# Kernel optimization log

Measured on AMD Instinct MI355X. Metric: run time of the kernel, lower is better.

The kernel has to match this reference:

```python
import jax, jax.numpy as jnp
import numpy as np

R = 6            # search radius
P = 2 * R + 1    # patch size = 13
D = 4            # mask downsample rate
TOPK = 36        # top-k over patch dim (eval path)


def _corr(fq, fm):
    """Local correlation volume (SpatialCorrelationSampler, kernel=1, patch=P).
    fq, fm: [b,c,h,w] -> [b, P*P, h*w]."""
    b, c, h, w = fq.shape
    fmp = jnp.pad(fm, ((0, 0), (0, 0), (R, R), (R, R)))
    rows = []
    for di in range(P):
        for dj in range(P):
            rows.append(jnp.einsum('bchw,bchw->bhw', fq, fmp[:, :, di:di + h, dj:dj + w]))
    return jnp.stack(rows, 1).reshape(b, P * P, h * w)


def _unfold(msk):
    """F.unfold(msk, kernel_size=P, padding=R): [b,o,h,w] -> [b,o,P*P,h*w]."""
    b, o, h, w = msk.shape
    mp = jnp.pad(msk, ((0, 0), (0, 0), (R, R), (R, R)))
    pats = [mp[:, :, di:di + h, dj:dj + w] for di in range(P) for dj in range(P)]
    return jnp.stack(pats, 2).reshape(b, o, P * P, h * w)


def _forward(feat_query, feat_mem0, feat_mem1, msk_mem0, msk_mem1):
    b, c, h, w = feat_query.shape
    # correlation volumes for each memory frame, concat over patch dim
    corr = jnp.concatenate([_corr(feat_query, feat_mem0),
                            _corr(feat_query, feat_mem1)], axis=1)
    corr = corr / jnp.sqrt(jnp.asarray(c, corr.dtype))          # [b, 2*P*P, N]
    # eval path: top-k over the (frames*P*P) patch axis, per pixel
    corr_t = corr.transpose(0, 2, 1)                              # [b, N, 2PP]
    vals, idx = jax.lax.top_k(corr_t, TOPK)                       # [b, N, K]
    wts = jax.nn.softmax(vals, axis=-1)                           # [b, N, K]
    # downsample masks by strided slicing, unfold, concat over patch dim
    msk = jnp.concatenate([_unfold(msk_mem0[:, :, ::D, ::D]),
                           _unfold(msk_mem1[:, :, ::D, ::D])], axis=2)  # [b,o,2PP,N]
    msk_t = msk.transpose(0, 3, 1, 2)                             # [b, N, o, 2PP]
    g = jnp.take_along_axis(msk_t, idx[:, :, None, :], axis=3)    # [b, N, o, K]
    out = (wts[:, :, None, :] * g).sum(-1)                        # [b, N, o]
    obj = msk_mem0.shape[1]
    return out.transpose(0, 2, 1).reshape(b, obj, h, w)


def setup_inputs() -> dict:
    key = jax.random.key(0)
    k = jax.random.split(key, 5)
    b, c, h, w = 1, 256, 120, 216
    obj = 11
    return {
        'feat_query': jax.random.normal(k[0], (b, c, h, w), jnp.float32),
        'feat_mem0': jax.random.normal(k[1], (b, c, h, w), jnp.float32),
        'feat_mem1': jax.random.normal(k[2], (b, c, h, w), jnp.float32),
        'msk_mem0': jax.random.uniform(k[3], (b, obj, h * D, w * D), jnp.float32),
        'msk_mem1': jax.random.uniform(k[4], (b, obj, h * D, w * D), jnp.float32),
    }


def reference(feat_query, feat_mem0, feat_mem1, msk_mem0, msk_mem1):
    return _forward(feat_query, feat_mem0, feat_mem1, msk_mem0, msk_mem1)
```

## Files before the change

kernel.cpp:

```cpp
#include <hip/hip_runtime.h>
#include <hip/hip_bf16.h>
#include <math.h>

#define H 120
#define W 216
#define C 256
#define NPIX (H*W)
#define PATCH 13
#define PP 169
#define RAD 6
#define TOPKN 36
#define OBJ 11
#define MD 4
#define CW 344

typedef unsigned short ushort;
typedef unsigned int   uint;
typedef __attribute__((ext_vector_type(8))) __bf16 bf16x8;
typedef __attribute__((ext_vector_type(4))) float   f32x4;

#define PLANE_B ((size_t)NPIX * 512)

#define YT 8
#define RT 20
#define XT 16
#define UW 32
#define PXS 128
#define ROWS (UW * PXS)
#define BUFB (RT * ROWS)
#define NXT 14
#define NYT 15
#define NWG (NXT * 2 * NYT)

__device__ inline ushort f2bf_rne(float x) {
  uint u = __float_as_uint(x);
  uint r = (u + 0x7FFFu + ((u >> 16) & 1u)) >> 16;
  return (ushort)r;
}
__device__ inline float bf2f(ushort h) { return __uint_as_float(((uint)h) << 16); }

__global__ __launch_bounds__(256) void k_prep(const float* __restrict__ fq,
                      const float* __restrict__ fm0, const float* __restrict__ fm1,
                      char* fqt, char* fm0t, char* fm1t) {
  const float* src = (blockIdx.z == 0) ? fq : (blockIdx.z == 1) ? fm0 : fm1;
  char* dst = (blockIdx.z == 0) ? fqt : (blockIdx.z == 1) ? fm0t : fm1t;

  const int p0 = blockIdx.x * 64;
  const int c0 = blockIdx.y * 64;
  const int tid = threadIdx.x;

  __shared__ float ts[64 * 65];
  {
    int p = tid & 63, cl = tid >> 6;
    #pragma unroll
    for (int jj = 0; jj < 16; ++jj) {
      int c = 4 * jj + cl;
      ts[c * 65 + p] = src[(size_t)(c0 + c) * NPIX + p0 + p];
    }
  }
  __syncthreads();
  {
    int pl = tid >> 2, sub = tid & 3;
    ushort hb[16], lb[16];
    #pragma unroll
    for (int i = 0; i < 16; ++i) {
      float x = ts[(sub * 16 + i) * 65 + pl];
      ushort h = f2bf_rne(x);
      hb[i] = h;
      lb[i] = f2bf_rne(x - bf2f(h));
    }
    size_t off = (size_t)(p0 + pl) * 512 + (size_t)c0 * 2 + sub * 32;
    *(uint4*)(dst + off)            = ((uint4*)hb)[0];
    *(uint4*)(dst + off + 16)       = ((uint4*)hb)[1];
    *(uint4*)(dst + PLANE_B + off)      = ((uint4*)lb)[0];
    *(uint4*)(dst + PLANE_B + off + 16) = ((uint4*)lb)[1];
  }
}

__global__ void k_downsample(const float* __restrict__ m0, const float* __restrict__ m1,
                             float* __restrict__ mds) {
  int i = blockIdx.x * 256 + threadIdx.x;
  const int total = 2 * OBJ * NPIX;
  if (i >= total) return;
  int fo = i / NPIX;
  int pix = i - fo * NPIX;
  int f = fo / OBJ, o = fo - f * OBJ;
  int y = pix / W, x = pix - y * W;
  const float* src = f ? m1 : m0;
  mds[i] = src[(size_t)o * (H*MD) * (W*MD) + (size_t)(MD*y) * (W*MD) + MD*x];
}

__global__ __launch_bounds__(1024, 4) void k_corr_mfma(const char* __restrict__ fqt,
                        const char* __restrict__ fm0t, const char* __restrict__ fm1t,
                        float* __restrict__ corr) {
  int b = blockIdx.x;
  int xcd = b & 7;
  int wgid = ((xcd < 4) ? xcd * 53 : 4 * 53 + (xcd - 4) * 52) + (b >> 3);
  int yt   = wgid % NYT;
  int rest = wgid / NYT;
  int f    = rest & 1;
  int xt   = rest >> 1;

  const int y0 = yt * YT;
  const int X0 = xt * XT;
  const int tid  = threadIdx.x;
  const int wv   = tid >> 6;
  const int wyy  = wv >> 1;
  const int nt   = wv & 1;
  const int lane = tid & 63;
  const int l15  = lane & 15, l4 = lane >> 4;
  const int y    = y0 + wyy;

  const char* frame = f ? fm1t : fm0t;

  __shared__ __align__(16) char bsm[2 * BUFB];

  const char* gsrc[5];
  #pragma unroll
  for (int i = 0; i < 5; ++i) {
    int gdest = wv * 64 + lane + 1024 * i;
    int ri  = gdest >> 8;
    int rem = gdest & 255;
    int px  = rem >> 3;
    int pqp = rem & 7;
    int pqs = pqp ^ (px & 7);
    int p   = pqs >> 2, q = pqs & 3;
    int r = y0 - 6 + ri;  r = (r < 0) ? 0 : (r >= H ? H - 1 : r);
    int u = X0 - 8 + px;  u = (u < 0) ? 0 : (u >= W ? W - 1 : u);
    gsrc[i] = frame + (size_t)p * PLANE_B + (size_t)(r * W + u) * 512 + q * 16;
  }

  int xA = X0 + l15;
  const char* pa = fqt + (size_t)(y * W + (xA < W ? xA : W - 1)) * 512 + l4 * 16;

  const int pxn = 16 * nt + l15;
  const uint sw  = (uint)((l15 & 7) << 4);
  const uint bh_off = (uint)((pxn * PXS +      l4 * 16) ^ sw);
  const uint bl_off = (uint)((pxn * PXS + 64 + l4 * 16) ^ sw);

  int u0 = X0 + 16 * nt + l15 - 8;
  bool uok = (u0 >= 0) && (u0 < W);

  f32x4 acc[13];
  #pragma unroll
  for (int di = 0; di < 13; ++di) acc[di] = (f32x4){0.f, 0.f, 0.f, 0.f};

  auto STAGE = [&](int buf, int kc) {
    #pragma unroll
    for (int i = 0; i < 5; ++i)
      __builtin_amdgcn_global_load_lds(
        (const __attribute__((address_space(1))) void*)(gsrc[i] + kc * 64),
        (__attribute__((address_space(3))) void*)(bsm + buf * BUFB + wv * 1024 + i * 16384),
        16, 0, 0);
  };

  STAGE(0, 0);
  uint4 aCh = *(const uint4*)(pa);
  uint4 aCl = *(const uint4*)(pa + PLANE_B);
  uint4 aNh, aNl;
  __syncthreads();

  #pragma unroll
  for (int kc = 0; kc < 8; ++kc) {
    if (kc < 7) {
      STAGE((kc + 1) & 1, kc + 1);
      aNh = *(const uint4*)(pa + (kc + 1) * 64);
      aNl = *(const uint4*)(pa + PLANE_B + (kc + 1) * 64);
    }
    const char* bb = bsm + (kc & 1) * BUFB;
    bf16x8 Ahv = __builtin_bit_cast(bf16x8, aCh);
    bf16x8 Alv = __builtin_bit_cast(bf16x8, aCl);

    #pragma unroll
    for (int di = 0; di < 13; ++di) {
      int rr = y + di - RAD;
      if (rr >= 0 && rr < H) {
        const char* rb = bb + (wyy + di) * ROWS;
        bf16x8 Bhv = *(const bf16x8*)(rb + bh_off);
        bf16x8 Blv = *(const bf16x8*)(rb + bl_off);
        acc[di] = __builtin_amdgcn_mfma_f32_16x16x32_bf16(Ahv, Bhv, acc[di], 0, 0, 0);
        acc[di] = __builtin_amdgcn_mfma_f32_16x16x32_bf16(Ahv, Blv, acc[di], 0, 0, 0);
        acc[di] = __builtin_amdgcn_mfma_f32_16x16x32_bf16(Alv, Bhv, acc[di], 0, 0, 0);
      }
    }
    aCh = aNh; aCl = aNl;
    __syncthreads();
  }

  float* cb = corr + (size_t)(y * W) * CW + f * PP;
  #pragma unroll
  for (int di = 0; di < 13; ++di) {
    #pragma unroll
    for (int j = 0; j < 4; ++j) {
      int m  = l4 * 4 + j;
      int x  = X0 + m;
      int dj = 16 * nt + l15 - m - 2;
      if (x < W && dj >= 0 && dj < PATCH)
        cb[(size_t)x * CW + di * PATCH + dj] = uok ? acc[di][j] * 0.0625f : 0.f;
    }
  }
}

__global__ __launch_bounds__(64) void k_corr_valu(const float* __restrict__ fq,
                       const float* __restrict__ fm0, const float* __restrict__ fm1,
                       float* __restrict__ corr) {
  int b = blockIdx.x;
  int lb = (b & 7) * 390 + (b >> 3);
  int y   = lb / 26;
  int r26 = lb - y * 26;
  int f   = r26 / 13;
  int di  = r26 - f * 13;
  const int tid = threadIdx.x;
  const int xg  = tid;
  const int r   = y + di - RAD;

  float* corr_base = corr + (size_t)(y * W) * CW + (f * PP + di * PATCH);

  if (r < 0 || r >= H) {
    if (xg < 54) {
      float* cp = corr_base + (size_t)(4 * xg) * CW;
      #pragma unroll
      for (int sub = 0; sub < 4; ++sub) {
        #pragma unroll
        for (int dj = 0; dj < PATCH; ++dj) cp[(size_t)sub * CW + dj] = 0.f;
      }
    }
    return;
  }

  const float* fm = f ? fm1 : fm0;
  __shared__ float fm_s[4 * 232];

  const float* pf[4];
  int  ldsoff[4];
  bool sval[4], mval[4];
  #pragma unroll
  for (int s = 0; s < 4; ++s) {
    int i = tid + 64 * s;
    sval[s] = (i < 232);
    int ii = sval[s] ? i : 0;
    int ch = ii / 58;
    int m  = ii - ch * 58;
    int x  = 4 * m - 8;
    mval[s] = sval[s] && (m >= 2) && (m <= 55);
    ldsoff[s] = ch * 232 + 4 * m;
    pf[s] = fm + (size_t)ch * NPIX + (size_t)r * W + (mval[s] ? x : 0);
  }

  const float* pq = fq + (size_t)y * W + 4 * ((xg < 54) ? xg : 0);

  float4 acc[PATCH];
  #pragma unroll
  for (int d = 0; d < PATCH; ++d) acc[d] = make_float4(0.f, 0.f, 0.f, 0.f);

  for (int c0 = 0; c0 < C; c0 += 4) {
    #pragma unroll
    for (int s = 0; s < 4; ++s) {
      if (sval[s]) {
        float4 v = make_float4(0.f, 0.f, 0.f, 0.f);
        if (mval[s]) v = *(const float4*)(pf[s]);
        *(float4*)&fm_s[ldsoff[s]] = v;
        pf[s] += 4 * (size_t)NPIX;
      }
    }
    __syncthreads();
    if (xg < 54) {
      #pragma unroll
      for (int ch = 0; ch < 4; ++ch) {
        float4 q4 = *(const float4*)(pq + (size_t)ch * NPIX);
        float rv[20];
        #pragma unroll
        for (int qq = 0; qq < 5; ++qq) {
          float4 t4 = *(const float4*)&fm_s[ch * 232 + 4 * xg + 4 * qq];
          rv[4*qq+0] = t4.x; rv[4*qq+1] = t4.y; rv[4*qq+2] = t4.z; rv[4*qq+3] = t4.w;
        }
        #pragma unroll
        for (int dj = 0; dj < PATCH; ++dj) {
          acc[dj].x += q4.x * rv[dj + 2];
          acc[dj].y += q4.y * rv[dj + 3];
          acc[dj].z += q4.z * rv[dj + 4];
          acc[dj].w += q4.w * rv[dj + 5];
        }
      }
      pq += 4 * (size_t)NPIX;
    }
    __syncthreads();
  }

  if (xg < 54) {
    float* cp = corr_base + (size_t)(4 * xg) * CW;
    #pragma unroll
    for (int dj = 0; dj < PATCH; ++dj) {
      cp[dj]                  = acc[dj].x * 0.0625f;
      cp[(size_t)1 * CW + dj] = acc[dj].y * 0.0625f;
      cp[(size_t)2 * CW + dj] = acc[dj].z * 0.0625f;
      cp[(size_t)3 * CW + dj] = acc[dj].w * 0.0625f;
    }
  }
}

__global__ __launch_bounds__(256) void k_topk(const float* __restrict__ corr,
                       const float* __restrict__ mds, float* __restrict__ out) {
  int wid = (blockIdx.x * 256 + threadIdx.x) >> 6;
  int lane = threadIdx.x & 63;
  if (wid >= NPIX) return;
  const float* cr = corr + (size_t)wid * CW;

  float v[6]; uint ui[6];
  #pragma unroll
  for (int s = 0; s < 6; ++s) {
    int idx = lane + 64 * s;
    bool ok = idx < 2 * PP;
    float f = ok ? cr[idx] : 0.f;
    v[s] = f;
    uint bb = __float_as_uint(f);
    uint u = bb ^ (uint)(((int)bb >> 31) | 0x80000000);
    ui[s] = ok ? u : 0u;
  }

  uint blo = 0u, bhi = 0xFFFFFFFFu;
  for (int it = 0; it < 32; ++it) {
    uint mid = blo + ((bhi - blo) >> 1);
    int c = 0;
    #pragma unroll
    for (int s = 0; s < 6; ++s)
      c += __popcll(__ballot(ui[s] > mid));
    if (c <= 35) bhi = mid; else blo = mid + 1;
  }
  const uint x0 = blo;

  int c_gt = 0;
  #pragma unroll
  for (int s = 0; s < 6; ++s) c_gt += __popcll(__ballot(ui[s] > x0));
  const int need = 36 - c_gt;

  uint tb = (x0 & 0x80000000u) ? (x0 ^ 0x80000000u) : ~x0;
  const float tf = __uint_as_float(tb);

  float w[6];
  float zp = 0.f;
  int prior = 0;
  #pragma unroll
  for (int s = 0; s < 6; ++s) {
    unsigned long long tie = __ballot(ui[s] == x0);
    uint below = __builtin_amdgcn_mbcnt_hi((uint)(tie >> 32),
                  __builtin_amdgcn_mbcnt_lo((uint)tie, 0u));
    bool acc = (ui[s] > x0) || ((ui[s] == x0) && ((prior + (int)below) < need));
    prior += __popcll(tie);
    w[s] = acc ? __expf(v[s] - tf) : 0.f;
    zp += w[s];
  }
  float Z = zp;
  #pragma unroll
  for (int off = 32; off >= 1; off >>= 1) Z += __shfl_xor(Z, off, 64);

  int y = wid / W, x = wid - (wid / W) * W;
  float no[OBJ];
  #pragma unroll
  for (int o = 0; o < OBJ; ++o) no[o] = 0.f;
  #pragma unroll
  for (int s = 0; s < 6; ++s) {
    if (w[s] > 0.f) {
      int idx = lane + 64 * s;
      int ff = idx >= PP;
      int r = idx - ff * PP;
      int di = r / PATCH, dj = r - (r / PATCH) * PATCH;
      int yy = y + di - RAD, xx = x + dj - RAD;
      if (yy >= 0 && yy < H && xx >= 0 && xx < W) {
        const float* mb = mds + ((size_t)ff * OBJ) * NPIX + yy * W + xx;
        #pragma unroll
        for (int o = 0; o < OBJ; ++o) no[o] += w[s] * mb[(size_t)o * NPIX];
      }
    }
  }
  float inv = 1.f / Z;
  #pragma unroll
  for (int o = 0; o < OBJ; ++o) {
    float p = no[o];
    #pragma unroll
    for (int off = 32; off >= 1; off >>= 1) p += __shfl_xor(p, off, 64);
    if (lane == 0) out[(size_t)o * NPIX + wid] = p * inv;
  }
}

extern "C" void kernel_launch(void* const* d_in, const int* in_sizes, int n_in,
                              void* d_out, int out_size, void* d_ws, size_t ws_size,
                              hipStream_t stream) {
  const float* fq  = (const float*)d_in[0];
  const float* fm0 = (const float*)d_in[1];
  const float* fm1 = (const float*)d_in[2];
  const float* m0  = (const float*)d_in[3];
  const float* m1  = (const float*)d_in[4];
  float* out = (float*)d_out;

  char* ws = (char*)d_ws;
  size_t off = 0;
  auto alloc = [&](size_t sz) { size_t o = off; off = (off + sz + 1023) & ~(size_t)1023; return o; };

  size_t mds_o  = alloc((size_t)2 * OBJ * NPIX * sizeof(float));
  size_t corr_o = alloc((size_t)NPIX * CW * sizeof(float));
  size_t fqt_o  = alloc(2 * PLANE_B);
  size_t fm0t_o = alloc(2 * PLANE_B);
  size_t fm1t_o = alloc(2 * PLANE_B);
  size_t needed = off;

  float* mds  = (float*)(ws + mds_o);
  float* corr = (float*)(ws + corr_o);

  k_downsample<<<(2 * OBJ * NPIX + 255) / 256, 256, 0, stream>>>(m0, m1, mds);

  if (ws_size >= needed) {
    char* fqt  = ws + fqt_o;
    char* fm0t = ws + fm0t_o;
    char* fm1t = ws + fm1t_o;
    dim3 gp(405, 4, 3);
    k_prep<<<gp, 256, 0, stream>>>(fq, fm0, fm1, fqt, fm0t, fm1t);
    k_corr_mfma<<<NWG, 1024, 0, stream>>>(fqt, fm0t, fm1t, corr);
  } else {
    k_corr_valu<<<120 * 26, 64, 0, stream>>>(fq, fm0, fm1, corr);
  }

  k_topk<<<NPIX / 4, 256, 0, stream>>>(corr, mds, out);
}
```

Before: 134.1 us.

## Compute two query rows per wave in correlation MFMA kernel to reuse B loads

Each wave now handles two adjacent query rows instead of one, so the block shrinks from 1024 to 512 threads. Every B fragment read from LDS for one memory row feeds both accumulator sets, which cuts LDS reads per MFMA roughly in half. Each wave also issues twice as many global-to-LDS staging loads. The cost is double the accumulator registers (26 f32x4), lower occupancy via launch bounds (512,2), and fewer waves per block to hide latency.

```diff
diff --git a/kernel.cpp b/kernel.cpp
--- a/kernel.cpp
+++ b/kernel.cpp
@@ -90,7 +90,7 @@
   mds[i] = src[(size_t)o * (H*MD) * (W*MD) + (size_t)(MD*y) * (W*MD) + MD*x];
 }
 
-__global__ __launch_bounds__(1024, 4) void k_corr_mfma(const char* __restrict__ fqt,
+__global__ __launch_bounds__(512, 2) void k_corr_mfma(const char* __restrict__ fqt,
                         const char* __restrict__ fm0t, const char* __restrict__ fm1t,
                         float* __restrict__ corr) {
   int b = blockIdx.x;
@@ -105,33 +105,34 @@
   const int X0 = xt * XT;
   const int tid  = threadIdx.x;
   const int wv   = tid >> 6;
-  const int wyy  = wv >> 1;
+  const int p    = wv >> 1;
   const int nt   = wv & 1;
   const int lane = tid & 63;
   const int l15  = lane & 15, l4 = lane >> 4;
-  const int y    = y0 + wyy;
+  const int ya   = y0 + 2 * p;
 
   const char* frame = f ? fm1t : fm0t;
 
   __shared__ __align__(16) char bsm[2 * BUFB];
 
-  const char* gsrc[5];
-  #pragma unroll
-  for (int i = 0; i < 5; ++i) {
-    int gdest = wv * 64 + lane + 1024 * i;
+  const char* gsrc[10];
+  #pragma unroll
+  for (int i = 0; i < 10; ++i) {
+    int gdest = wv * 640 + i * 64 + lane;
     int ri  = gdest >> 8;
     int rem = gdest & 255;
     int px  = rem >> 3;
     int pqp = rem & 7;
     int pqs = pqp ^ (px & 7);
-    int p   = pqs >> 2, q = pqs & 3;
+    int pp  = pqs >> 2, q = pqs & 3;
     int r = y0 - 6 + ri;  r = (r < 0) ? 0 : (r >= H ? H - 1 : r);
     int u = X0 - 8 + px;  u = (u < 0) ? 0 : (u >= W ? W - 1 : u);
-    gsrc[i] = frame + (size_t)p * PLANE_B + (size_t)(r * W + u) * 512 + q * 16;
+    gsrc[i] = frame + (size_t)pp * PLANE_B + (size_t)(r * W + u) * 512 + q * 16;
   }
 
   int xA = X0 + l15;
-  const char* pa = fqt + (size_t)(y * W + (xA < W ? xA : W - 1)) * 512 + l4 * 16;
+  const char* pa0 = fqt + (size_t)(ya * W + (xA < W ? xA : W - 1)) * 512 + l4 * 16;
+  const char* pa1 = pa0 + (size_t)W * 512;
 
   const int pxn = 16 * nt + l15;
   const uint sw  = (uint)((l15 & 7) << 4);
@@ -141,53 +142,70 @@
   int u0 = X0 + 16 * nt + l15 - 8;
   bool uok = (u0 >= 0) && (u0 < W);
 
-  f32x4 acc[13];
-  #pragma unroll
-  for (int di = 0; di < 13; ++di) acc[di] = (f32x4){0.f, 0.f, 0.f, 0.f};
+  f32x4 acc0[13], acc1[13];
+  #pragma unroll
+  for (int di = 0; di < 13; ++di) {
+    acc0[di] = (f32x4){0.f, 0.f, 0.f, 0.f};
+    acc1[di] = (f32x4){0.f, 0.f, 0.f, 0.f};
+  }
 
   auto STAGE = [&](int buf, int kc) {
     #pragma unroll
-    for (int i = 0; i < 5; ++i)
+    for (int i = 0; i < 10; ++i)
       __builtin_amdgcn_global_load_lds(
         (const __attribute__((address_space(1))) void*)(gsrc[i] + kc * 64),
-        (__attribute__((address_space(3))) void*)(bsm + buf * BUFB + wv * 1024 + i * 16384),
+        (__attribute__((address_space(3))) void*)(bsm + buf * BUFB + wv * 10240 + i * 1024),
         16, 0, 0);
   };
 
   STAGE(0, 0);
-  uint4 aCh = *(const uint4*)(pa);
-  uint4 aCl = *(const uint4*)(pa + PLANE_B);
-  uint4 aNh, aNl;
+  uint4 aC0h = *(const uint4*)(pa0);
+  uint4 aC0l = *(const uint4*)(pa0 + PLANE_B);
+  uint4 aC1h = *(const uint4*)(pa1);
+  uint4 aC1l = *(const uint4*)(pa1 + PLANE_B);
+  uint4 aN0h, aN0l, aN1h, aN1l;
   __syncthreads();
 
   #pragma unroll
   for (int kc = 0; kc < 8; ++kc) {
     if (kc < 7) {
       STAGE((kc + 1) & 1, kc + 1);
-      aNh = *(const uint4*)(pa + (kc + 1) * 64);
-      aNl = *(const uint4*)(pa + PLANE_B + (kc + 1) * 64);
+      aN0h = *(const uint4*)(pa0 + (kc + 1) * 64);
+      aN0l = *(const uint4*)(pa0 + PLANE_B + (kc + 1) * 64);
+      aN1h = *(const uint4*)(pa1 + (kc + 1) * 64);
+      aN1l = *(const uint4*)(pa1 + PLANE_B + (kc + 1) * 64);
     }
     const char* bb = bsm + (kc & 1) * BUFB;
-    bf16x8 Ahv = __builtin_bit_cast(bf16x8, aCh);
-    bf16x8 Alv = __builtin_bit_cast(bf16x8, aCl);
-
-    #pragma unroll
-    for (int di = 0; di < 13; ++di) {
-      int rr = y + di - RAD;
-      if (rr >= 0 && rr < H) {
-        const char* rb = bb + (wyy + di) * ROWS;
+    bf16x8 A0h = __builtin_bit_cast(bf16x8, aC0h);
+    bf16x8 A0l = __builtin_bit_cast(bf16x8, aC0l);
+    bf16x8 A1h = __builtin_bit_cast(bf16x8, aC1h);
+    bf16x8 A1l = __builtin_bit_cast(bf16x8, aC1l);
+
+    #pragma unroll
+    for (int ri = 0; ri < 14; ++ri) {
+      int row = ya + ri - RAD;
+      if (row >= 0 && row < H) {
+        const char* rb = bb + (2 * p + ri) * ROWS;
         bf16x8 Bhv = *(const bf16x8*)(rb + bh_off);
         bf16x8 Blv = *(const bf16x8*)(rb + bl_off);
-        acc[di] = __builtin_amdgcn_mfma_f32_16x16x32_bf16(Ahv, Bhv, acc[di], 0, 0, 0);
-        acc[di] = __builtin_amdgcn_mfma_f32_16x16x32_bf16(Ahv, Blv, acc[di], 0, 0, 0);
-        acc[di] = __builtin_amdgcn_mfma_f32_16x16x32_bf16(Alv, Bhv, acc[di], 0, 0, 0);
-      }
-    }
-    aCh = aNh; aCl = aNl;
+        if (ri <= 12) {
+          acc0[ri] = __builtin_amdgcn_mfma_f32_16x16x32_bf16(A0h, Bhv, acc0[ri], 0, 0, 0);
+          acc0[ri] = __builtin_amdgcn_mfma_f32_16x16x32_bf16(A0h, Blv, acc0[ri], 0, 0, 0);
+          acc0[ri] = __builtin_amdgcn_mfma_f32_16x16x32_bf16(A0l, Bhv, acc0[ri], 0, 0, 0);
+        }
+        if (ri >= 1) {
+          acc1[ri-1] = __builtin_amdgcn_mfma_f32_16x16x32_bf16(A1h, Bhv, acc1[ri-1], 0, 0, 0);
+          acc1[ri-1] = __builtin_amdgcn_mfma_f32_16x16x32_bf16(A1h, Blv, acc1[ri-1], 0, 0, 0);
+          acc1[ri-1] = __builtin_amdgcn_mfma_f32_16x16x32_bf16(A1l, Bhv, acc1[ri-1], 0, 0, 0);
+        }
+      }
+    }
+    aC0h = aN0h; aC0l = aN0l; aC1h = aN1h; aC1l = aN1l;
     __syncthreads();
   }
 
-  float* cb = corr + (size_t)(y * W) * CW + f * PP;
+  float* cb0 = corr + (size_t)(ya * W) * CW + f * PP;
+  float* cb1 = cb0 + (size_t)W * CW;
   #pragma unroll
   for (int di = 0; di < 13; ++di) {
     #pragma unroll
@@ -195,8 +213,10 @@
       int m  = l4 * 4 + j;
       int x  = X0 + m;
       int dj = 16 * nt + l15 - m - 2;
-      if (x < W && dj >= 0 && dj < PATCH)
-        cb[(size_t)x * CW + di * PATCH + dj] = uok ? acc[di][j] * 0.0625f : 0.f;
+      if (x < W && dj >= 0 && dj < PATCH) {
+        cb0[(size_t)x * CW + di * PATCH + dj] = uok ? acc0[di][j] * 0.0625f : 0.f;
+        cb1[(size_t)x * CW + di * PATCH + dj] = uok ? acc1[di][j] * 0.0625f : 0.f;
+      }
     }
   }
 }
@@ -376,10 +396,10 @@
   float inv = 1.f / Z;
   #pragma unroll
   for (int o = 0; o < OBJ; ++o) {
-    float p = no[o];
-    #pragma unroll
-    for (int off = 32; off >= 1; off >>= 1) p += __shfl_xor(p, off, 64);
-    if (lane == 0) out[(size_t)o * NPIX + wid] = p * inv;
+    float pr = no[o];
+    #pragma unroll
+    for (int off = 32; off >= 1; off >>= 1) pr += __shfl_xor(pr, off, 64);
+    if (lane == 0) out[(size_t)o * NPIX + wid] = pr * inv;
   }
 }
 
@@ -415,7 +435,7 @@
     char* fm1t = ws + fm1t_o;
     dim3 gp(405, 4, 3);
     k_prep<<<gp, 256, 0, stream>>>(fq, fm0, fm1, fqt, fm0t, fm1t);
-    k_corr_mfma<<<NWG, 1024, 0, stream>>>(fqt, fm0t, fm1t, corr);
+    k_corr_mfma<<<NWG, 512, 0, stream>>>(fqt, fm0t, fm1t, corr);
   } else {
     k_corr_valu<<<120 * 26, 64, 0, stream>>>(fq, fm0, fm1, corr);
   }
```

Measured after the change: 138.3 us. 1.03x slower.

## Process both memory frames per workgroup and use two-stage radix top-k threshold search

Applied to the files above, without the earlier changes.

The correlation kernel now loops over both memory frames inside one workgroup, halving the grid to 210 workgroups. It pipelines the frame-1 staging behind the frame-0 compute and reuses the query A-operand addressing. The XCD remapping is adjusted for the smaller grid. The top-k kernel first does a 16-iteration binary search on the upper 16 bits of the key and only falls back to a full-precision refinement when ties straddle the threshold, cutting the per-pixel ballot loop count in the common case. Risks are lower occupancy and parallelism for the correlation stage (210 blocks across 256 CUs) and divergence in the fallback path.

```diff
diff --git a/kernel.cpp b/kernel.cpp
--- a/kernel.cpp
+++ b/kernel.cpp
@@ -30,7 +30,7 @@
 #define BUFB (RT * ROWS)
 #define NXT 14
 #define NYT 15
-#define NWG (NXT * 2 * NYT)
+#define NWG2 (NXT * NYT)
 
 __device__ inline ushort f2bf_rne(float x) {
   uint u = __float_as_uint(x);
@@ -94,12 +94,10 @@
                         const char* __restrict__ fm0t, const char* __restrict__ fm1t,
                         float* __restrict__ corr) {
   int b = blockIdx.x;
-  int xcd = b & 7;
-  int wgid = ((xcd < 4) ? xcd * 53 : 4 * 53 + (xcd - 4) * 52) + (b >> 3);
+  int xcd = b & 7, idx = b >> 3;
+  int wgid = (xcd < 2) ? xcd * 27 + idx : 54 + (xcd - 2) * 26 + idx;
   int yt   = wgid % NYT;
-  int rest = wgid / NYT;
-  int f    = rest & 1;
-  int xt   = rest >> 1;
+  int xt   = wgid / NYT;
 
   const int y0 = yt * YT;
   const int X0 = xt * XT;
@@ -111,11 +109,12 @@
   const int l15  = lane & 15, l4 = lane >> 4;
   const int y    = y0 + wyy;
 
-  const char* frame = f ? fm1t : fm0t;
-
   __shared__ __align__(16) char bsm[2 * BUFB];
 
-  const char* gsrc[5];
+  uint soff[5];
+  uint ldst;
+  {
+  }
   #pragma unroll
   for (int i = 0; i < 5; ++i) {
     int gdest = wv * 64 + lane + 1024 * i;
@@ -127,8 +126,9 @@
     int p   = pqs >> 2, q = pqs & 3;
     int r = y0 - 6 + ri;  r = (r < 0) ? 0 : (r >= H ? H - 1 : r);
     int u = X0 - 8 + px;  u = (u < 0) ? 0 : (u >= W ? W - 1 : u);
-    gsrc[i] = frame + (size_t)p * PLANE_B + (size_t)(r * W + u) * 512 + q * 16;
-  }
+    soff[i] = (uint)((size_t)p * PLANE_B + (size_t)(r * W + u) * 512 + q * 16);
+  }
+  ldst = (uint)(wv * 1024 + lane * 16);
 
   int xA = X0 + l15;
   const char* pa = fqt + (size_t)(y * W + (xA < W ? xA : W - 1)) * 512 + l4 * 16;
@@ -145,58 +145,65 @@
   #pragma unroll
   for (int di = 0; di < 13; ++di) acc[di] = (f32x4){0.f, 0.f, 0.f, 0.f};
 
-  auto STAGE = [&](int buf, int kc) {
+  auto STAGE = [&](int buf, const char* fb, int kn) {
     #pragma unroll
     for (int i = 0; i < 5; ++i)
       __builtin_amdgcn_global_load_lds(
-        (const __attribute__((address_space(1))) void*)(gsrc[i] + kc * 64),
-        (__attribute__((address_space(3))) void*)(bsm + buf * BUFB + wv * 1024 + i * 16384),
+        (const __attribute__((address_space(1))) void*)(fb + soff[i] + kn * 64),
+        (__attribute__((address_space(3))) void*)(bsm + buf * BUFB + ldst + i * 16384),
         16, 0, 0);
   };
 
-  STAGE(0, 0);
+  STAGE(0, fm0t, 0);
   uint4 aCh = *(const uint4*)(pa);
   uint4 aCl = *(const uint4*)(pa + PLANE_B);
   uint4 aNh, aNl;
   __syncthreads();
 
   #pragma unroll
-  for (int kc = 0; kc < 8; ++kc) {
-    if (kc < 7) {
-      STAGE((kc + 1) & 1, kc + 1);
-      aNh = *(const uint4*)(pa + (kc + 1) * 64);
-      aNl = *(const uint4*)(pa + PLANE_B + (kc + 1) * 64);
-    }
-    const char* bb = bsm + (kc & 1) * BUFB;
-    bf16x8 Ahv = __builtin_bit_cast(bf16x8, aCh);
-    bf16x8 Alv = __builtin_bit_cast(bf16x8, aCl);
-
+  for (int fi = 0; fi < 2; ++fi) {
+    #pragma unroll
+    for (int kc = 0; kc < 8; ++kc) {
+      int t = fi * 8 + kc;
+      if (t < 15) {
+        const char* sfb = (t < 7) ? fm0t : fm1t;
+        int kn = (kc + 1) & 7;
+        STAGE((kc + 1) & 1, sfb, kn);
+        aNh = *(const uint4*)(pa + kn * 64);
+        aNl = *(const uint4*)(pa + PLANE_B + kn * 64);
+      }
+      const char* bb = bsm + (kc & 1) * BUFB;
+      bf16x8 Ahv = __builtin_bit_cast(bf16x8, aCh);
+      bf16x8 Alv = __builtin_bit_cast(bf16x8, aCl);
+
+      #pragma unroll
+      for (int di = 0; di < 13; ++di) {
+        int rr = y + di - RAD;
+        if (rr >= 0 && rr < H) {
+          const char* rb = bb + (wyy + di) * ROWS;
+          bf16x8 Bhv = *(const bf16x8*)(rb + bh_off);
+          bf16x8 Blv = *(const bf16x8*)(rb + bl_off);
+          acc[di] = __builtin_amdgcn_mfma_f32_16x16x32_bf16(Ahv, Bhv, acc[di], 0, 0, 0);
+          acc[di] = __builtin_amdgcn_mfma_f32_16x16x32_bf16(Ahv, Blv, acc[di], 0, 0, 0);
+          acc[di] = __builtin_amdgcn_mfma_f32_16x16x32_bf16(Alv, Bhv, acc[di], 0, 0, 0);
+        }
+      }
+      aCh = aNh; aCl = aNl;
+      __syncthreads();
+    }
+
+    float* cb = corr + (size_t)(y * W) * CW + fi * PP;
     #pragma unroll
     for (int di = 0; di < 13; ++di) {
-      int rr = y + di - RAD;
-      if (rr >= 0 && rr < H) {
-        const char* rb = bb + (wyy + di) * ROWS;
-        bf16x8 Bhv = *(const bf16x8*)(rb + bh_off);
-        bf16x8 Blv = *(const bf16x8*)(rb + bl_off);
-        acc[di] = __builtin_amdgcn_mfma_f32_16x16x32_bf16(Ahv, Bhv, acc[di], 0, 0, 0);
-        acc[di] = __builtin_amdgcn_mfma_f32_16x16x32_bf16(Ahv, Blv, acc[di], 0, 0, 0);
-        acc[di] = __builtin_amdgcn_mfma_f32_16x16x32_bf16(Alv, Bhv, acc[di], 0, 0, 0);
-      }
-    }
-    aCh = aNh; aCl = aNl;
-    __syncthreads();
-  }
-
-  float* cb = corr + (size_t)(y * W) * CW + f * PP;
-  #pragma unroll
-  for (int di = 0; di < 13; ++di) {
-    #pragma unroll
-    for (int j = 0; j < 4; ++j) {
-      int m  = l4 * 4 + j;
-      int x  = X0 + m;
-      int dj = 16 * nt + l15 - m - 2;
-      if (x < W && dj >= 0 && dj < PATCH)
-        cb[(size_t)x * CW + di * PATCH + dj] = uok ? acc[di][j] * 0.0625f : 0.f;
+      #pragma unroll
+      for (int j = 0; j < 4; ++j) {
+        int m  = l4 * 4 + j;
+        int x  = X0 + m;
+        int dj = 16 * nt + l15 - m - 2;
+        if (x < W && dj >= 0 && dj < PATCH)
+          cb[(size_t)x * CW + di * PATCH + dj] = uok ? acc[di][j] * 0.0625f : 0.f;
+      }
+      acc[di] = (f32x4){0.f, 0.f, 0.f, 0.f};
     }
   }
 }
@@ -318,38 +325,68 @@
     ui[s] = ok ? u : 0u;
   }
 
-  uint blo = 0u, bhi = 0xFFFFFFFFu;
-  for (int it = 0; it < 32; ++it) {
-    uint mid = blo + ((bhi - blo) >> 1);
+  uint lo = 0u, hi = 0xFFFFu;
+  for (int it = 0; it < 16; ++it) {
+    uint mid = (lo + hi) >> 1;
     int c = 0;
     #pragma unroll
     for (int s = 0; s < 6; ++s)
-      c += __popcll(__ballot(ui[s] > mid));
-    if (c <= 35) bhi = mid; else blo = mid + 1;
-  }
-  const uint x0 = blo;
-
-  int c_gt = 0;
-  #pragma unroll
-  for (int s = 0; s < 6; ++s) c_gt += __popcll(__ballot(ui[s] > x0));
-  const int need = 36 - c_gt;
-
-  uint tb = (x0 & 0x80000000u) ? (x0 ^ 0x80000000u) : ~x0;
-  const float tf = __uint_as_float(tb);
+      c += __popcll(__ballot((ui[s] >> 16) > mid));
+    if (c <= 35) hi = mid; else lo = mid + 1;
+  }
+  const uint k16 = lo;
+
+  int g = 0, e = 0;
+  #pragma unroll
+  for (int s = 0; s < 6; ++s) {
+    g += __popcll(__ballot((ui[s] >> 16) > k16));
+    e += __popcll(__ballot((ui[s] >> 16) == k16));
+  }
+  const int need = 36 - g;
 
   float w[6];
   float zp = 0.f;
-  int prior = 0;
-  #pragma unroll
-  for (int s = 0; s < 6; ++s) {
-    unsigned long long tie = __ballot(ui[s] == x0);
-    uint below = __builtin_amdgcn_mbcnt_hi((uint)(tie >> 32),
-                  __builtin_amdgcn_mbcnt_lo((uint)tie, 0u));
-    bool acc = (ui[s] > x0) || ((ui[s] == x0) && ((prior + (int)below) < need));
-    prior += __popcll(tie);
-    w[s] = acc ? __expf(v[s] - tf) : 0.f;
-    zp += w[s];
-  }
+
+  if (e == need) {
+    uint x0 = k16 << 16;
+    uint tb = (x0 & 0x80000000u) ? (x0 ^ 0x80000000u) : ~x0;
+    const float tf = __uint_as_float(tb);
+    #pragma unroll
+    for (int s = 0; s < 6; ++s) {
+      bool a = (ui[s] >> 16) >= k16;
+      w[s] = a ? __expf(v[s] - tf) : 0.f;
+      zp += w[s];
+    }
+  } else {
+    uint l2 = k16 << 16, h2 = (k16 << 16) | 0xFFFFu;
+    for (int it = 0; it < 16; ++it) {
+      uint mid = l2 + ((h2 - l2) >> 1);
+      int c = 0;
+      #pragma unroll
+      for (int s = 0; s < 6; ++s)
+        c += __popcll(__ballot(ui[s] > mid));
+      if (c <= 35) h2 = mid; else l2 = mid + 1;
+    }
+    const uint x0 = l2;
+    int cgt = 0;
+    #pragma unroll
+    for (int s = 0; s < 6; ++s) cgt += __popcll(__ballot(ui[s] > x0));
+    const int needT = 36 - cgt;
+    uint tb = (x0 & 0x80000000u) ? (x0 ^ 0x80000000u) : ~x0;
+    const float tf = __uint_as_float(tb);
+    int prior = 0;
+    #pragma unroll
+    for (int s = 0; s < 6; ++s) {
+      unsigned long long tie = __ballot(ui[s] == x0);
+      uint below = __builtin_amdgcn_mbcnt_hi((uint)(tie >> 32),
+                    __builtin_amdgcn_mbcnt_lo((uint)tie, 0u));
+      bool a = (ui[s] > x0) || ((ui[s] == x0) && ((prior + (int)below) < needT));
+      prior += __popcll(tie);
+      w[s] = a ? __expf(v[s] - tf) : 0.f;
+      zp += w[s];
+    }
+  }
+
   float Z = zp;
   #pragma unroll
   for (int off = 32; off >= 1; off >>= 1) Z += __shfl_xor(Z, off, 64);
@@ -376,10 +413,10 @@
   float inv = 1.f / Z;
   #pragma unroll
   for (int o = 0; o < OBJ; ++o) {
-    float p = no[o];
-    #pragma unroll
-    for (int off = 32; off >= 1; off >>= 1) p += __shfl_xor(p, off, 64);
-    if (lane == 0) out[(size_t)o * NPIX + wid] = p * inv;
+    float pr = no[o];
+    #pragma unroll
+    for (int off = 32; off >= 1; off >>= 1) pr += __shfl_xor(pr, off, 64);
+    if (lane == 0) out[(size_t)o * NPIX + wid] = pr * inv;
   }
 }
 
@@ -415,7 +452,7 @@
     char* fm1t = ws + fm1t_o;
     dim3 gp(405, 4, 3);
     k_prep<<<gp, 256, 0, stream>>>(fq, fm0, fm1, fqt, fm0t, fm1t);
-    k_corr_mfma<<<NWG, 1024, 0, stream>>>(fqt, fm0t, fm1t, corr);
+    k_corr_mfma<<<NWG2, 1024, 0, stream>>>(fqt, fm0t, fm1t, corr);
   } else {
     k_corr_valu<<<120 * 26, 64, 0, stream>>>(fq, fm0, fm1, corr);
   }
```

New measurement: 127.2 us. -5.2%, faster.
